# Kernel optimization log

Hardware: AMD Instinct MI355X
Metric: run time of the kernel (lower is better)

Reference implementation:

```python
import jax, jax.numpy as jnp
import numpy as np

KERNEL_SIZE = 3

def setup_inputs() -> dict:
    key = jax.random.key(0)
    k1, k2, k3, k4, k5 = jax.random.split(key, 5)
    B, L, D, K = 4, 4096, 1024, KERNEL_SIZE
    x = jax.random.normal(k1, (B, L, D), dtype=jnp.float32)
    # depthwise conv: torch weight shape (D, 1, K) -> store as (D, K)
    fan_dw = 1.0 / np.sqrt(1 * K)
    w_dw = jax.random.uniform(k2, (D, K), dtype=jnp.float32, minval=-fan_dw, maxval=fan_dw)
    b_dw = jax.random.uniform(k3, (D,), dtype=jnp.float32, minval=-fan_dw, maxval=fan_dw)
    # pointwise conv: torch weight shape (D, D, 1) -> store as (D_out, D_in)
    fan_pw = 1.0 / np.sqrt(D * 1)
    w_pw = jax.random.uniform(k4, (D, D), dtype=jnp.float32, minval=-fan_pw, maxval=fan_pw)
    b_pw = jax.random.uniform(k5, (D,), dtype=jnp.float32, minval=-fan_pw, maxval=fan_pw)
    return {"x": x, "w_dw": w_dw, "b_dw": b_dw, "w_pw": w_pw, "b_pw": b_pw}

def _causal_dw_pw(x, w_dw, b_dw, w_pw, b_pw):
    # x: (B, L, D); causal left-pad by K-1 along L
    K = w_dw.shape[1]
    L = x.shape[1]
    xp = jnp.pad(x, ((0, 0), (K - 1, 0), (0, 0)))  # (B, L+K-1, D)
    # depthwise: y[b,l,d] = sum_k xp[b,l+k,d] * w_dw[d,k]
    y = sum(xp[:, k:k + L, :] * w_dw[:, k] for k in range(K)) + b_dw
    # pointwise 1x1 conv: mix channels
    return jnp.einsum('bld,ed->ble', y, w_pw) + b_pw

def reference(x, w_dw, b_dw, w_pw, b_pw):
    return _causal_dw_pw(x, w_dw, b_dw, w_pw, b_pw)
```

## Files before the change

kernel.cpp:

```cpp
#include <hip/hip_runtime.h>
#include <hip/hip_bf16.h>
#include <stdint.h>

#define B_SZ   4
#define L_SEQ  4096
#define D_DIM  1024
#define M_TOT  (B_SZ * L_SEQ)

typedef __bf16 bf16;
typedef __attribute__((ext_vector_type(8))) __bf16 bf16x8;
typedef __attribute__((ext_vector_type(4))) float   f32x4;

#define GLOAD_LDS16(g, l)                                                     \
  __builtin_amdgcn_global_load_lds(                                           \
      (const __attribute__((address_space(1))) void*)(g),                     \
      (__attribute__((address_space(3))) void*)(l), 16, 0, 0)

__global__ __launch_bounds__(256) void dw_bf16_kernel(
    const float* __restrict__ x, const float* __restrict__ w_dw,
    const float* __restrict__ b_dw, bf16* __restrict__ y,
    const float* __restrict__ w_pw, bf16* __restrict__ wpwb) {
  const int t = threadIdx.x;
  if (blockIdx.x >= B_SZ * (L_SEQ / 16)) {
    int i = ((blockIdx.x - B_SZ * (L_SEQ / 16)) * 256 + t) * 8;
    float4 a = *(const float4*)(w_pw + i);
    float4 b = *(const float4*)(w_pw + i + 4);
    union { bf16 h[8]; int4 v; } r;
    r.h[0] = (bf16)a.x; r.h[1] = (bf16)a.y; r.h[2] = (bf16)a.z; r.h[3] = (bf16)a.w;
    r.h[4] = (bf16)b.x; r.h[5] = (bf16)b.y; r.h[6] = (bf16)b.z; r.h[7] = (bf16)b.w;
    *(int4*)(wpwb + i) = r.v;
    return;
  }
  const int b  = blockIdx.x >> 8;
  const int l0 = (blockIdx.x & 255) * 16;
  const int d0 = t * 4;
  const float* xb = x + (size_t)b * L_SEQ * D_DIM + d0;
  bf16*        yb = y + (size_t)b * L_SEQ * D_DIM + d0;

  float4 xr[18];
  const float4 zero = make_float4(0.f, 0.f, 0.f, 0.f);
  xr[0] = (l0 >= 2) ? *(const float4*)(xb + (size_t)(l0 - 2) * D_DIM) : zero;
  xr[1] = (l0 >= 1) ? *(const float4*)(xb + (size_t)(l0 - 1) * D_DIM) : zero;
#pragma unroll
  for (int j = 0; j < 16; ++j)
    xr[j + 2] = *(const float4*)(xb + (size_t)(l0 + j) * D_DIM);

  const float* wp = w_dw + d0 * 3;
  float4 wa = *(const float4*)(wp);
  float4 wb = *(const float4*)(wp + 4);
  float4 wc = *(const float4*)(wp + 8);
  float4 bv = *(const float4*)(b_dw + d0);

#pragma unroll
  for (int j = 0; j < 16; ++j) {
    float4 x2 = xr[j], x1 = xr[j + 1], x0 = xr[j + 2];
    float a0 = fmaf(x2.x, wa.x, fmaf(x1.x, wa.y, fmaf(x0.x, wa.z, bv.x)));
    float a1 = fmaf(x2.y, wa.w, fmaf(x1.y, wb.x, fmaf(x0.y, wb.y, bv.y)));
    float a2 = fmaf(x2.z, wb.z, fmaf(x1.z, wb.w, fmaf(x0.z, wc.x, bv.z)));
    float a3 = fmaf(x2.w, wc.y, fmaf(x1.w, wc.z, fmaf(x0.w, wc.w, bv.w)));
    union { bf16 h[4]; int2 v; } o;
    o.h[0] = (bf16)a0; o.h[1] = (bf16)a1; o.h[2] = (bf16)a2; o.h[3] = (bf16)a3;
    *(int2*)(yb + (size_t)(l0 + j) * D_DIM) = o.v;
  }
}

#define BM 128
#define BN 128
#define BK 64
#define EP_ROWP 68

__global__ __launch_bounds__(256, 4) void gemm_bt_kernel(
    const bf16* __restrict__ A,
    const bf16* __restrict__ Bm,
    const float* __restrict__ bias, float* __restrict__ C) {
  __shared__ __align__(16) char smem[32768];

  const int t    = threadIdx.x;
  const int m0   = blockIdx.x * BM;
  const int n0   = blockIdx.y * BN;
  const int lane = t & 63;
  const int wv   = t >> 6;
  const int wm   = (wv >> 1) * 64;
  const int wn   = (wv & 1) * 64;
  const int lrow = lane & 15;
  const int q    = lane >> 4;

  f32x4 acc[4][4] = {};

  int goff[4];
#pragma unroll
  for (int i = 0; i < 4; ++i) {
    int s   = i * 256 + t;
    int row = s >> 3;
    int gc  = (s & 7) ^ (row & 7);
    goff[i] = row * (D_DIM * 2) + gc * 16;
  }
  const char* pA = (const char*)(A  + (size_t)m0 * D_DIM);
  const char* pB = (const char*)(Bm + (size_t)n0 * D_DIM);
  const unsigned lbase = (unsigned)(wv * 1024);

  int aoff[4], boff[4];
#pragma unroll
  for (int i = 0; i < 4; ++i) {
    int mrow = wm + i * 16 + lrow;
    aoff[i] = mrow * 128 + ((q ^ (mrow & 7)) * 16);
    int nrow = wn + i * 16 + lrow;
    boff[i] = 16384 + nrow * 128 + ((q ^ (nrow & 7)) * 16);
  }

  for (int it = 0; it < D_DIM / BK; ++it) {
    __syncthreads();
#pragma unroll
    for (int i = 0; i < 4; ++i) {
      unsigned off = (unsigned)(i * 4096) + lbase;
      GLOAD_LDS16(pA + goff[i], smem + off);
      GLOAD_LDS16(pB + goff[i], smem + 16384 + off);
    }
    pA += BK * 2;
    pB += BK * 2;
    __syncthreads();

#pragma unroll
    for (int kk = 0; kk < 2; ++kk) {
      const int x = kk * 64;
      bf16x8 af[4], bfr[4];
#pragma unroll
      for (int i = 0; i < 4; ++i) {
        af[i]  = *(const bf16x8*)(smem + (aoff[i] ^ x));
        bfr[i] = *(const bf16x8*)(smem + (boff[i] ^ x));
      }
#pragma unroll
      for (int i = 0; i < 4; ++i)
#pragma unroll
        for (int j = 0; j < 4; ++j)
          acc[i][j] = __builtin_amdgcn_mfma_f32_16x16x32_bf16(af[i], bfr[j], acc[i][j], 0, 0, 0);
    }
  }

  __syncthreads();
  float* ep = (float*)smem + (size_t)wv * (16 * EP_ROWP);

  float bvj[4];
#pragma unroll
  for (int j = 0; j < 4; ++j) bvj[j] = bias[n0 + wn + j * 16 + lrow];

#pragma unroll
  for (int i = 0; i < 4; ++i) {
#pragma unroll
    for (int j = 0; j < 4; ++j)
#pragma unroll
      for (int r = 0; r < 4; ++r)
        ep[(q * 4 + r) * EP_ROWP + j * 16 + lrow] = acc[i][j][r] + bvj[j];
#pragma unroll
    for (int s = 0; s < 4; ++s) {
      int flat = s * 64 + lane;
      int row  = flat >> 4;
      int c4   = flat & 15;
      float4 v = *(const float4*)(ep + row * EP_ROWP + c4 * 4);
      int gm = m0 + wm + i * 16 + row;
      int gn = n0 + wn + c4 * 4;
      *(float4*)(C + (size_t)gm * D_DIM + gn) = v;
    }
  }
}

__global__ __launch_bounds__(256) void fallback_kernel(
    const float* __restrict__ x, const float* __restrict__ w_dw,
    const float* __restrict__ b_dw, const float* __restrict__ w_pw,
    const float* __restrict__ b_pw, float* __restrict__ out) {
  __shared__ float ys[D_DIM];
  const int m = blockIdx.x;
  const int l = m & (L_SEQ - 1);
  const int t = threadIdx.x;
  const float* xr = x + (size_t)m * D_DIM;
#pragma unroll
  for (int c = 0; c < 4; ++c) {
    int d = t + c * 256;
    float a = fmaf(xr[d], w_dw[d * 3 + 2], b_dw[d]);
    if (l >= 1) a = fmaf(xr[d - D_DIM], w_dw[d * 3 + 1], a);
    if (l >= 2) a = fmaf(xr[d - 2 * D_DIM], w_dw[d * 3 + 0], a);
    ys[d] = a;
  }
  __syncthreads();
#pragma unroll
  for (int c = 0; c < 4; ++c) {
    int e = t + c * 256;
    const float* wr = w_pw + (size_t)e * D_DIM;
    float a = b_pw[e];
    for (int d = 0; d < D_DIM; ++d) a = fmaf(ys[d], wr[d], a);
    out[(size_t)m * D_DIM + e] = a;
  }
}

extern "C" void kernel_launch(void* const* d_in, const int* in_sizes, int n_in,
                              void* d_out, int out_size, void* d_ws, size_t ws_size,
                              hipStream_t stream) {
  (void)in_sizes; (void)n_in; (void)out_size;
  const float* x    = (const float*)d_in[0];
  const float* w_dw = (const float*)d_in[1];
  const float* b_dw = (const float*)d_in[2];
  const float* w_pw = (const float*)d_in[3];
  const float* b_pw = (const float*)d_in[4];
  float* out = (float*)d_out;

  const size_t y_elems = (size_t)M_TOT * D_DIM;
  const size_t w_elems = (size_t)D_DIM * D_DIM;
  const size_t need = (y_elems + w_elems) * sizeof(bf16);

  if (ws_size >= need) {
    bf16* y    = (bf16*)d_ws;
    bf16* wpwb = (bf16*)d_ws + y_elems;
    const int dw_blocks  = B_SZ * (L_SEQ / 16);
    const int cvt_blocks = (D_DIM * D_DIM / 8) / 256;
    dw_bf16_kernel<<<dw_blocks + cvt_blocks, 256, 0, stream>>>(x, w_dw, b_dw, y, w_pw, wpwb);
    dim3 grid(M_TOT / BM, D_DIM / BN);
    gemm_bt_kernel<<<grid, 256, 0, stream>>>(y, wpwb, b_pw, out);
  } else {
    fallback_kernel<<<M_TOT, 256, 0, stream>>>(x, w_dw, b_dw, w_pw, b_pw, out);
  }
}
```

Before: 173.5 us.

## Fuse depthwise conv into GEMM A-tile load, drop bf16 intermediate buffer

Computes the causal depthwise conv directly inside the GEMM k-loop. Each block loads fp32 x rows with a two-row halo, applies the 3-tap filter and writes bf16 A tiles into swizzled LDS, replacing the separate y round-trip through global memory. The weight conversion stays as a small standalone kernel. The cost is that every N-block column (8 of them) recomputes the conv and reads fp32 x, which is twice the bytes of the old bf16 y. Register pressure also rises (launch bounds lowered to 3), and the A loads become synchronous register loads rather than async global-to-LDS.

```diff
diff --git a/kernel.cpp b/kernel.cpp
--- a/kernel.cpp
+++ b/kernel.cpp
@@ -16,52 +16,15 @@
       (const __attribute__((address_space(1))) void*)(g),                     \
       (__attribute__((address_space(3))) void*)(l), 16, 0, 0)
 
-__global__ __launch_bounds__(256) void dw_bf16_kernel(
-    const float* __restrict__ x, const float* __restrict__ w_dw,
-    const float* __restrict__ b_dw, bf16* __restrict__ y,
-    const float* __restrict__ w_pw, bf16* __restrict__ wpwb) {
-  const int t = threadIdx.x;
-  if (blockIdx.x >= B_SZ * (L_SEQ / 16)) {
-    int i = ((blockIdx.x - B_SZ * (L_SEQ / 16)) * 256 + t) * 8;
-    float4 a = *(const float4*)(w_pw + i);
-    float4 b = *(const float4*)(w_pw + i + 4);
-    union { bf16 h[8]; int4 v; } r;
-    r.h[0] = (bf16)a.x; r.h[1] = (bf16)a.y; r.h[2] = (bf16)a.z; r.h[3] = (bf16)a.w;
-    r.h[4] = (bf16)b.x; r.h[5] = (bf16)b.y; r.h[6] = (bf16)b.z; r.h[7] = (bf16)b.w;
-    *(int4*)(wpwb + i) = r.v;
-    return;
-  }
-  const int b  = blockIdx.x >> 8;
-  const int l0 = (blockIdx.x & 255) * 16;
-  const int d0 = t * 4;
-  const float* xb = x + (size_t)b * L_SEQ * D_DIM + d0;
-  bf16*        yb = y + (size_t)b * L_SEQ * D_DIM + d0;
-
-  float4 xr[18];
-  const float4 zero = make_float4(0.f, 0.f, 0.f, 0.f);
-  xr[0] = (l0 >= 2) ? *(const float4*)(xb + (size_t)(l0 - 2) * D_DIM) : zero;
-  xr[1] = (l0 >= 1) ? *(const float4*)(xb + (size_t)(l0 - 1) * D_DIM) : zero;
-#pragma unroll
-  for (int j = 0; j < 16; ++j)
-    xr[j + 2] = *(const float4*)(xb + (size_t)(l0 + j) * D_DIM);
-
-  const float* wp = w_dw + d0 * 3;
-  float4 wa = *(const float4*)(wp);
-  float4 wb = *(const float4*)(wp + 4);
-  float4 wc = *(const float4*)(wp + 8);
-  float4 bv = *(const float4*)(b_dw + d0);
-
-#pragma unroll
-  for (int j = 0; j < 16; ++j) {
-    float4 x2 = xr[j], x1 = xr[j + 1], x0 = xr[j + 2];
-    float a0 = fmaf(x2.x, wa.x, fmaf(x1.x, wa.y, fmaf(x0.x, wa.z, bv.x)));
-    float a1 = fmaf(x2.y, wa.w, fmaf(x1.y, wb.x, fmaf(x0.y, wb.y, bv.y)));
-    float a2 = fmaf(x2.z, wb.z, fmaf(x1.z, wb.w, fmaf(x0.z, wc.x, bv.z)));
-    float a3 = fmaf(x2.w, wc.y, fmaf(x1.w, wc.z, fmaf(x0.w, wc.w, bv.w)));
-    union { bf16 h[4]; int2 v; } o;
-    o.h[0] = (bf16)a0; o.h[1] = (bf16)a1; o.h[2] = (bf16)a2; o.h[3] = (bf16)a3;
-    *(int2*)(yb + (size_t)(l0 + j) * D_DIM) = o.v;
-  }
+__global__ __launch_bounds__(256) void cvt_bf16_kernel(
+    const float* __restrict__ w, bf16* __restrict__ o) {
+  int i = (blockIdx.x * 256 + threadIdx.x) * 8;
+  float4 a = *(const float4*)(w + i);
+  float4 b = *(const float4*)(w + i + 4);
+  union { bf16 h[8]; int4 v; } r;
+  r.h[0] = (bf16)a.x; r.h[1] = (bf16)a.y; r.h[2] = (bf16)a.z; r.h[3] = (bf16)a.w;
+  r.h[4] = (bf16)b.x; r.h[5] = (bf16)b.y; r.h[6] = (bf16)b.z; r.h[7] = (bf16)b.w;
+  *(int4*)(o + i) = r.v;
 }
 
 #define BM 128
@@ -69,10 +32,13 @@
 #define BK 64
 #define EP_ROWP 68
 
-__global__ __launch_bounds__(256, 4) void gemm_bt_kernel(
-    const bf16* __restrict__ A,
-    const bf16* __restrict__ Bm,
-    const float* __restrict__ bias, float* __restrict__ C) {
+__global__ __launch_bounds__(256, 3) void fused_dw_gemm_kernel(
+    const float* __restrict__ x,
+    const float* __restrict__ w_dw,
+    const float* __restrict__ b_dw,
+    const bf16* __restrict__ Bw,
+    const float* __restrict__ bias,
+    float* __restrict__ C) {
   __shared__ __align__(16) char smem[32768];
 
   const int t    = threadIdx.x;
@@ -87,17 +53,27 @@
 
   f32x4 acc[4][4] = {};
 
-  int goff[4];
+  int goffB[4];
 #pragma unroll
   for (int i = 0; i < 4; ++i) {
     int s   = i * 256 + t;
     int row = s >> 3;
     int gc  = (s & 7) ^ (row & 7);
-    goff[i] = row * (D_DIM * 2) + gc * 16;
-  }
-  const char* pA = (const char*)(A  + (size_t)m0 * D_DIM);
-  const char* pB = (const char*)(Bm + (size_t)n0 * D_DIM);
+    goffB[i] = row * (D_DIM * 2) + gc * 16;
+  }
+  const char* pB = (const char*)(Bw + (size_t)n0 * D_DIM);
   const unsigned lbase = (unsigned)(wv * 1024);
+
+  const int g  = t & 15;
+  const int rt = t >> 4;
+  const float* xp = x + (size_t)(m0 + rt * 8) * D_DIM + g * 4;
+  const bool halo_ok = ((m0 & (L_SEQ - 1)) != 0) || (rt != 0);
+  int awoff[8];
+#pragma unroll
+  for (int j = 0; j < 8; ++j) {
+    int m = rt * 8 + j;
+    awoff[j] = m * 128 + (((g >> 1) ^ (m & 7)) * 16) + ((g & 1) * 8);
+  }
 
   int aoff[4], boff[4];
 #pragma unroll
@@ -108,26 +84,51 @@
     boff[i] = 16384 + nrow * 128 + ((q ^ (nrow & 7)) * 16);
   }
 
+  const float4 zero = make_float4(0.f, 0.f, 0.f, 0.f);
+
   for (int it = 0; it < D_DIM / BK; ++it) {
+    const int k0 = it * BK;
     __syncthreads();
-#pragma unroll
-    for (int i = 0; i < 4; ++i) {
-      unsigned off = (unsigned)(i * 4096) + lbase;
-      GLOAD_LDS16(pA + goff[i], smem + off);
-      GLOAD_LDS16(pB + goff[i], smem + 16384 + off);
+
+#pragma unroll
+    for (int i = 0; i < 4; ++i)
+      GLOAD_LDS16(pB + goffB[i], smem + 16384 + (unsigned)(i * 4096) + lbase);
+
+    float4 xr[10];
+    xr[0] = halo_ok ? *(const float4*)(xp + k0 - 2 * D_DIM) : zero;
+    xr[1] = halo_ok ? *(const float4*)(xp + k0 - 1 * D_DIM) : zero;
+#pragma unroll
+    for (int h = 0; h < 8; ++h)
+      xr[h + 2] = *(const float4*)(xp + k0 + h * D_DIM);
+
+    const float* wq = w_dw + (size_t)(k0 + g * 4) * 3;
+    float4 wa = *(const float4*)(wq);
+    float4 wb = *(const float4*)(wq + 4);
+    float4 wc = *(const float4*)(wq + 8);
+    float4 bv = *(const float4*)(b_dw + k0 + g * 4);
+
+#pragma unroll
+    for (int j = 0; j < 8; ++j) {
+      float4 x2 = xr[j], x1 = xr[j + 1], x0 = xr[j + 2];
+      float a0 = fmaf(x2.x, wa.x, fmaf(x1.x, wa.y, fmaf(x0.x, wa.z, bv.x)));
+      float a1 = fmaf(x2.y, wa.w, fmaf(x1.y, wb.x, fmaf(x0.y, wb.y, bv.y)));
+      float a2 = fmaf(x2.z, wb.z, fmaf(x1.z, wb.w, fmaf(x0.z, wc.x, bv.z)));
+      float a3 = fmaf(x2.w, wc.y, fmaf(x1.w, wc.z, fmaf(x0.w, wc.w, bv.w)));
+      union { bf16 h[4]; int2 v; } o;
+      o.h[0] = (bf16)a0; o.h[1] = (bf16)a1; o.h[2] = (bf16)a2; o.h[3] = (bf16)a3;
+      *(int2*)(smem + awoff[j]) = o.v;
     }
-    pA += BK * 2;
     pB += BK * 2;
     __syncthreads();
 
 #pragma unroll
     for (int kk = 0; kk < 2; ++kk) {
-      const int x = kk * 64;
+      const int xo = kk * 64;
       bf16x8 af[4], bfr[4];
 #pragma unroll
       for (int i = 0; i < 4; ++i) {
-        af[i]  = *(const bf16x8*)(smem + (aoff[i] ^ x));
-        bfr[i] = *(const bf16x8*)(smem + (boff[i] ^ x));
+        af[i]  = *(const bf16x8*)(smem + (aoff[i] ^ xo));
+        bfr[i] = *(const bf16x8*)(smem + (boff[i] ^ xo));
       }
 #pragma unroll
       for (int i = 0; i < 4; ++i)
@@ -161,6 +162,7 @@
       int gn = n0 + wn + c4 * 4;
       *(float4*)(C + (size_t)gm * D_DIM + gn) = v;
     }
+    __syncthreads();
   }
 }
 
@@ -203,18 +205,12 @@
   const float* b_pw = (const float*)d_in[4];
   float* out = (float*)d_out;
 
-  const size_t y_elems = (size_t)M_TOT * D_DIM;
   const size_t w_elems = (size_t)D_DIM * D_DIM;
-  const size_t need = (y_elems + w_elems) * sizeof(bf16);
-
-  if (ws_size >= need) {
-    bf16* y    = (bf16*)d_ws;
-    bf16* wpwb = (bf16*)d_ws + y_elems;
-    const int dw_blocks  = B_SZ * (L_SEQ / 16);
-    const int cvt_blocks = (D_DIM * D_DIM / 8) / 256;
-    dw_bf16_kernel<<<dw_blocks + cvt_blocks, 256, 0, stream>>>(x, w_dw, b_dw, y, w_pw, wpwb);
+  if (ws_size >= w_elems * sizeof(bf16)) {
+    bf16* wpwb = (bf16*)d_ws;
+    cvt_bf16_kernel<<<(D_DIM * D_DIM / 8) / 256, 256, 0, stream>>>(w_pw, wpwb);
     dim3 grid(M_TOT / BM, D_DIM / BN);
-    gemm_bt_kernel<<<grid, 256, 0, stream>>>(y, wpwb, b_pw, out);
+    fused_dw_gemm_kernel<<<grid, 256, 0, stream>>>(x, w_dw, b_dw, wpwb, b_pw, out);
   } else {
     fallback_kernel<<<M_TOT, 256, 0, stream>>>(x, w_dw, b_dw, w_pw, b_pw, out);
   }
```

Result: slower. 247.6 us (+42.8%).
